# Kernel optimization log

Hardware: AMD Instinct MI355X
Metric: run time of the kernel (lower is better)

The kernel has to match this reference:

```python
import jax, jax.numpy as jnp
import numpy as np

S, B, H, NH = 2048, 1, 2048, 16
HD = H // NH
ROTARY_BASE = 10000.0
MASK_FILL = -10000.0  # gpt2_attention_mask_func fill value


def _rotate_half(x):
    x1, x2 = jnp.split(x, 2, axis=-1)
    return jnp.concatenate((-x2, x1), axis=-1)


def _rotary_cos_sin(seq_len, dim, dtype):
    inv_freq = 1.0 / (ROTARY_BASE ** (jnp.arange(0, dim, 2, dtype=jnp.float32) / dim))
    t = jnp.arange(seq_len, dtype=jnp.float32)
    freqs = t[:, None] * inv_freq[None, :]          # [s, dim/2]
    emb = jnp.concatenate((freqs, freqs), axis=-1)  # [s, dim]
    # shape [s, 1, 1, dim] to broadcast over (batch, heads)
    return jnp.cos(emb)[:, None, None, :].astype(dtype), jnp.sin(emb)[:, None, None, :].astype(dtype)


def setup_inputs() -> dict:
    key = jax.random.key(0)
    k0, k1, k2 = jax.random.split(key, 3)
    hidden_states = jax.random.normal(k0, (S, B, H), dtype=jnp.float32) * 0.02
    # causal mask: True = masked (upper triangle above diagonal)
    attention_mask = jnp.triu(jnp.ones((1, 1, S, S), dtype=bool), k=1)
    w_qkv = jax.random.normal(k1, (3 * H, H), dtype=jnp.float32) * 0.02
    b_qkv = jnp.zeros((3 * H,), dtype=jnp.float32)
    w_dense = jax.random.normal(k2, (H, H), dtype=jnp.float32) * 0.02
    return {"hidden_states": hidden_states, "attention_mask": attention_mask,
            "w_qkv": w_qkv, "b_qkv": b_qkv, "w_dense": w_dense}


def reference(hidden_states, attention_mask, w_qkv, b_qkv, w_dense):
    s, b, h = hidden_states.shape
    # fused QKV projection: [s, b, 3h]
    mixed = jnp.einsum('sbh,oh->sbo', hidden_states, w_qkv) + b_qkv
    mixed = mixed.reshape(s, b, NH, 3 * HD)
    q, k, v = jnp.split(mixed, 3, axis=-1)  # each [s, b, nh, hd]
    # rotary embedding (rotary_pct == 1 -> full head dim)
    cos, sin = _rotary_cos_sin(s, HD, q.dtype)
    q = q * cos + _rotate_half(q) * sin
    k = k * cos + _rotate_half(k) * sin
    # scaled QK^T: [b, nh, sq, sk]
    norm_factor = jnp.asarray(1.0 / np.sqrt(HD), dtype=q.dtype)
    scores = jnp.einsum('sbnd,tbnd->bnst', q, k) * norm_factor
    scores = jnp.where(attention_mask, jnp.asarray(MASK_FILL, scores.dtype), scores)
    probs = jax.nn.softmax(scores.astype(jnp.float32), axis=-1).astype(scores.dtype)
    # PV: [s, b, nh, hd]
    ctx = jnp.einsum('bnst,tbnd->sbnd', probs, v)
    ctx = ctx.reshape(s, b, h)
    # RowParallelLinear with skip_bias_add: bias returned separately (not added)
    out = jnp.einsum('sbh,oh->sbo', ctx, w_dense)
    return out
```

## Files before the change

### kernel.cpp

```cpp
#include <hip/hip_runtime.h>


#define S_LEN 2048
#define NHEAD 16
#define HDIM  128
#define HID   2048
#define H3    6144

typedef short bf16x8 __attribute__((ext_vector_type(8)));
typedef float f32x4  __attribute__((ext_vector_type(4)));

__device__ __forceinline__ float bf2f(ushort u) {
  union { float f; unsigned int i; } v; v.i = ((unsigned int)u) << 16; return v.f;
}
__device__ __forceinline__ ushort f2bf(float f) {
  union { float f; unsigned int i; } v; v.f = f;
  unsigned int r = v.i + 0x7fffu + ((v.i >> 16) & 1u);
  return (ushort)(r >> 16);
}
__device__ __forceinline__ int4 cvt8(const float* p) {
  float4 a = *(const float4*)p, b = *(const float4*)(p + 4);
  union { ushort u[8]; int4 v; } r;
  r.u[0] = f2bf(a.x); r.u[1] = f2bf(a.y); r.u[2] = f2bf(a.z); r.u[3] = f2bf(a.w);
  r.u[4] = f2bf(b.x); r.u[5] = f2bf(b.y); r.u[6] = f2bf(b.z); r.u[7] = f2bf(b.w);
  return r.v;
}

typedef __attribute__((address_space(1))) const unsigned int gu32;
typedef __attribute__((address_space(3))) unsigned int lu32;
__device__ __forceinline__ void async16(const void* g, void* l) {
  __builtin_amdgcn_global_load_lds((gu32*)g, (lu32*)l, 16, 0, 0);
}

__global__ __launch_bounds__(256) void cvt_bf16(const float* __restrict__ src,
                                                ushort* __restrict__ dst, int n8) {
  int i = blockIdx.x * 256 + threadIdx.x;
  if (i < n8) *(int4*)&dst[(size_t)i * 8] = cvt8(&src[(size_t)i * 8]);
}

template<int BM, int BN, bool HAS_BIAS, bool OUT_F32>
__global__ __launch_bounds__(256) void gemm_async(const ushort* __restrict__ A,
                                                  const ushort* __restrict__ W,
                                                  const float* __restrict__ bias,
                                                  void* __restrict__ Cv,
                                                  int N, int K, int AS, int AH) {
  __shared__ __align__(16) ushort As[BM * 32];
  __shared__ __align__(16) ushort Ws[BN * 32];
  const int tid  = threadIdx.x;
  const int lane = tid & 63;
  const int w    = tid >> 6;
  const int wr   = w >> 1, wc = w & 1;
  const int quad = lane >> 4, ln15 = lane & 15;
  const int tm = blockIdx.y * BM, tn = blockIdx.x * BN;
  constexpr int MI = BM / 32, NJ = BN / 32;

  f32x4 acc[MI][NJ];
#pragma unroll
  for (int i = 0; i < MI; ++i)
#pragma unroll
    for (int j = 0; j < NJ; ++j) acc[i][j] = (f32x4){0.f, 0.f, 0.f, 0.f};

  const int lrow = lane >> 2;
  const int lcol = (lane & 3) * 8;

  for (int k0 = 0; k0 < K; k0 += 32) {
    const int aoff = (k0 >> 7) * AH + (k0 & 127) + lcol;
    for (int r = w; r < (BM + BN) / 16; r += 4) {
      if (r < BM / 16) {
        async16(&A[(size_t)(tm + r * 16 + lrow) * AS + aoff], &As[r * 16 * 32]);
      } else {
        const int rb = r - BM / 16;
        async16(&W[(size_t)(tn + rb * 16 + lrow) * K + k0 + lcol], &Ws[rb * 16 * 32]);
      }
    }
    __syncthreads();
    bf16x8 af[MI], bw[NJ];
#pragma unroll
    for (int i = 0; i < MI; ++i)
      af[i] = *(const bf16x8*)&As[((BM / 2) * wr + 16 * i + ln15) * 32 + quad * 8];
#pragma unroll
    for (int j = 0; j < NJ; ++j)
      bw[j] = *(const bf16x8*)&Ws[((BN / 2) * wc + 16 * j + ln15) * 32 + quad * 8];
#pragma unroll
    for (int i = 0; i < MI; ++i)
#pragma unroll
      for (int j = 0; j < NJ; ++j)
        acc[i][j] = __builtin_amdgcn_mfma_f32_16x16x32_bf16(af[i], bw[j], acc[i][j], 0, 0, 0);
    __syncthreads();
  }

#pragma unroll
  for (int i = 0; i < MI; ++i)
#pragma unroll
    for (int j = 0; j < NJ; ++j) {
      int col = tn + (BN / 2) * wc + 16 * j + ln15;
      float badd = HAS_BIAS ? bias[col] : 0.0f;
#pragma unroll
      for (int r = 0; r < 4; ++r) {
        int row = tm + (BM / 2) * wr + 16 * i + 4 * quad + r;
        float val = acc[i][j][r] + badd;
        if (OUT_F32) ((float*)Cv)[(size_t)row * N + col] = val;
        else         ((ushort*)Cv)[(size_t)row * N + col] = f2bf(val);
      }
    }
}

template<bool A_F32, bool HAS_BIAS, bool OUT_F32>
__global__ __launch_bounds__(256) void gemm_bt(const void* __restrict__ Av,
                                               const float* __restrict__ W,
                                               const float* __restrict__ bias,
                                               void* __restrict__ Cv,
                                               int M, int N, int K, int AS, int AH) {
  __shared__ __align__(16) ushort As[128 * 40];
  __shared__ __align__(16) ushort Ws[128 * 40];
  const int tid  = threadIdx.x;
  const int lane = tid & 63;
  const int w    = tid >> 6;
  const int wr   = w >> 1, wc = w & 1;
  const int quad = lane >> 4, ln15 = lane & 15;
  const int tm = blockIdx.y * 128, tn = blockIdx.x * 128;

  f32x4 acc[4][4];
#pragma unroll
  for (int i = 0; i < 4; ++i)
#pragma unroll
    for (int j = 0; j < 4; ++j) acc[i][j] = (f32x4){0.f, 0.f, 0.f, 0.f};

  const int row0 = tid >> 2, row1 = row0 + 64;
  const int kp   = (tid & 3) * 8;

  for (int k0 = 0; k0 < K; k0 += 32) {
    const int ka   = k0 + kp;
    const int aoff = (ka >> 7) * AH + (ka & 127);
    if (A_F32) {
      const float* A = (const float*)Av;
      *(int4*)&As[row0 * 40 + kp] = cvt8(&A[(size_t)(tm + row0) * AS + aoff]);
      *(int4*)&As[row1 * 40 + kp] = cvt8(&A[(size_t)(tm + row1) * AS + aoff]);
    } else {
      const ushort* A = (const ushort*)Av;
      *(int4*)&As[row0 * 40 + kp] = *(const int4*)&A[(size_t)(tm + row0) * AS + aoff];
      *(int4*)&As[row1 * 40 + kp] = *(const int4*)&A[(size_t)(tm + row1) * AS + aoff];
    }
    *(int4*)&Ws[row0 * 40 + kp] = cvt8(&W[(size_t)(tn + row0) * K + ka]);
    *(int4*)&Ws[row1 * 40 + kp] = cvt8(&W[(size_t)(tn + row1) * K + ka]);
    __syncthreads();
    bf16x8 af[4], bw[4];
#pragma unroll
    for (int i = 0; i < 4; ++i)
      af[i] = *(const bf16x8*)&As[(64 * wr + 16 * i + ln15) * 40 + quad * 8];
#pragma unroll
    for (int j = 0; j < 4; ++j)
      bw[j] = *(const bf16x8*)&Ws[(64 * wc + 16 * j + ln15) * 40 + quad * 8];
#pragma unroll
    for (int i = 0; i < 4; ++i)
#pragma unroll
      for (int j = 0; j < 4; ++j)
        acc[i][j] = __builtin_amdgcn_mfma_f32_16x16x32_bf16(af[i], bw[j], acc[i][j], 0, 0, 0);
    __syncthreads();
  }

#pragma unroll
  for (int i = 0; i < 4; ++i)
#pragma unroll
    for (int j = 0; j < 4; ++j) {
      int col = tn + 64 * wc + 16 * j + ln15;
      float badd = HAS_BIAS ? bias[col] : 0.0f;
#pragma unroll
      for (int r = 0; r < 4; ++r) {
        int row = tm + 64 * wr + 16 * i + 4 * quad + r;
        float val = acc[i][j][r] + badd;
        if (OUT_F32) ((float*)Cv)[(size_t)row * N + col] = val;
        else         ((ushort*)Cv)[(size_t)row * N + col] = f2bf(val);
      }
    }
}

__global__ __launch_bounds__(256) void rope_kernel(ushort* __restrict__ mixed) {
  int t = blockIdx.x * 256 + threadIdx.x;
  int d = t & 63;
  int n = (t >> 6) & (NHEAD - 1);
  int s = t >> 10;
  ushort* base = mixed + (size_t)s * H3 + n * 384;
  float invf = exp2f((float)d * (-13.287712379549449f / 64.0f));
  float ang = (float)s * invf;
  float si, c; sincosf(ang, &si, &c);
  float q0 = bf2f(base[d]),       q1 = bf2f(base[64 + d]);
  float k0 = bf2f(base[128 + d]), k1 = bf2f(base[192 + d]);
  base[d]       = f2bf(q0 * c - q1 * si);
  base[64 + d]  = f2bf(q1 * c + q0 * si);
  base[128 + d] = f2bf(k0 * c - k1 * si);
  base[192 + d] = f2bf(k1 * c + k0 * si);
}

__global__ __launch_bounds__(256) void v_transpose(const ushort* __restrict__ mixed,
                                                   ushort* __restrict__ vt) {
  __shared__ __align__(16) ushort Vl[64 * 136];
  const int tid = threadIdx.x;
  const int sb = blockIdx.x;
  const int n  = blockIdx.y;
#pragma unroll
  for (int it = 0; it < 4; ++it) {
    int c = tid + it * 256;
    int row = c >> 4, dp = (c & 15) * 8;
    *(int4*)&Vl[row * 136 + dp] =
        *(const int4*)&mixed[(size_t)(sb * 64 + row) * H3 + n * 384 + 256 + dp];
  }
  __syncthreads();
#pragma unroll
  for (int it = 0; it < 4; ++it) {
    int c = tid + it * 256;
    int d = c >> 3, sp = (c & 7) * 8;
    union { ushort u[8]; int4 v; } pk;
#pragma unroll
    for (int e = 0; e < 8; ++e) pk.u[e] = Vl[(sp + e) * 136 + d];
    *(int4*)&vt[((size_t)(n * 128 + d)) * S_LEN + sb * 64 + sp] = pk.v;
  }
}

__global__ __launch_bounds__(256, 2) void attn_kernel(const ushort* __restrict__ mixed,
                                                      const ushort* __restrict__ vt,
                                                      ushort* __restrict__ ctx,
                                                      int CS, int CH) {
  __shared__ __align__(16) ushort Ks[2][64 * 128];
  __shared__ __align__(16) ushort Vs[128 * 64];
  __shared__ __align__(16) ushort Ss[4][16 * 72];

  const int tid  = threadIdx.x;
  const int lane = tid & 63;
  const int w    = tid >> 6;
  const int quad = lane >> 4, ln15 = lane & 15;
  const int qb = blockIdx.x;
  const int n  = blockIdx.y;
  const float scale = 0.08838834764831845f;

  const ushort* Kg = mixed + n * 384 + 128;
  const ushort* Vg = vt + (size_t)n * 128 * S_LEN;

  bf16x8 aqr[4];
#pragma unroll
  for (int ks = 0; ks < 4; ++ks)
    aqr[ks] = *(const bf16x8*)&mixed[(size_t)(qb * 64 + 16 * w + ln15) * H3 + n * 384
                                     + ks * 32 + quad * 8];

  f32x4 acc_o[8];
#pragma unroll
  for (int jt = 0; jt < 8; ++jt) acc_o[jt] = (f32x4){0.f, 0.f, 0.f, 0.f};
  float m_run[4], l_run[4];
#pragma unroll
  for (int r = 0; r < 4; ++r) { m_run[r] = -1e30f; l_run[r] = 0.0f; }

  ushort* Ssw = Ss[w];

  const int krow = lane >> 4, kcs = lane & 15;
  const int vrow = lane >> 3, vcs = lane & 7;
  const int swz  = ln15 & 7;

#define STAGE_K(KT, BUF)                                                        \
  { _Pragma("unroll")                                                           \
    for (int i = 0; i < 4; ++i) {                                               \
      int kr = w * 16 + i * 4 + krow;                                           \
      int kcl = kcs ^ (kr & 7);                                                 \
      async16(&Kg[(size_t)((KT) * 64 + kr) * H3 + kcl * 8],                     \
              &Ks[BUF][(w * 16 + i * 4) * 128]);                                \
    } }
#define STAGE_V(KT)                                                             \
  { _Pragma("unroll")                                                           \
    for (int i = 0; i < 4; ++i) {                                               \
      int vr = w * 32 + i * 8 + vrow;                                           \
      int vcl = vcs ^ (vr & 7);                                                 \
      async16(&Vg[(size_t)vr * S_LEN + (KT) * 64 + vcl * 8],                    \
              &Vs[(w * 32 + i * 8) * 64]);                                      \
    } }

  int cur = 0;
  STAGE_K(0, 0);
  __syncthreads();

  for (int kt = 0; kt <= qb; ++kt) {
    STAGE_V(kt);
    if (kt < qb) STAGE_K(kt + 1, cur ^ 1);

    f32x4 sacc[4];
#pragma unroll
    for (int jt = 0; jt < 4; ++jt) sacc[jt] = (f32x4){0.f, 0.f, 0.f, 0.f};
#pragma unroll
    for (int ks = 0; ks < 4; ++ks) {
#pragma unroll
      for (int jt = 0; jt < 4; ++jt) {
        bf16x8 bk = *(const bf16x8*)&Ks[cur][(16 * jt + ln15) * 128
                                            + ((ks * 4 + quad) ^ swz) * 8];
        sacc[jt] = __builtin_amdgcn_mfma_f32_16x16x32_bf16(aqr[ks], bk, sacc[jt], 0, 0, 0);
      }
    }

    float sv[4][4];
    const int ig = qb * 64 + 16 * w + 4 * quad;
#pragma unroll
    for (int jt = 0; jt < 4; ++jt) {
      int jg = kt * 64 + 16 * jt + ln15;
#pragma unroll
      for (int r = 0; r < 4; ++r) {
        float x = sacc[jt][r] * scale;
        sv[jt][r] = (jg > ig + r) ? -10000.0f : x;
      }
    }

    float tmx[4];
#pragma unroll
    for (int r = 0; r < 4; ++r)
      tmx[r] = fmaxf(fmaxf(sv[0][r], sv[1][r]), fmaxf(sv[2][r], sv[3][r]));
#pragma unroll
    for (int m = 1; m <= 8; m <<= 1)
#pragma unroll
      for (int r = 0; r < 4; ++r) tmx[r] = fmaxf(tmx[r], __shfl_xor(tmx[r], m));

    float alpha[4];
#pragma unroll
    for (int r = 0; r < 4; ++r) {
      float m_new = fmaxf(m_run[r], tmx[r]);
      alpha[r] = __expf(m_run[r] - m_new);
      m_run[r] = m_new;
    }

    float ps[4] = {0.f, 0.f, 0.f, 0.f};
#pragma unroll
    for (int jt = 0; jt < 4; ++jt)
#pragma unroll
      for (int r = 0; r < 4; ++r) {
        float p = __expf(sv[jt][r] - m_run[r]);
        Ssw[(4 * quad + r) * 72 + 16 * jt + ln15] = f2bf(p);
        ps[r] += p;
      }
#pragma unroll
    for (int m = 1; m <= 8; m <<= 1)
#pragma unroll
      for (int r = 0; r < 4; ++r) ps[r] += __shfl_xor(ps[r], m);
#pragma unroll
    for (int r = 0; r < 4; ++r) l_run[r] = alpha[r] * l_run[r] + ps[r];

#pragma unroll
    for (int jt = 0; jt < 8; ++jt)
#pragma unroll
      for (int r = 0; r < 4; ++r) acc_o[jt][r] *= alpha[r];

    __syncthreads();

#pragma unroll
    for (int ks = 0; ks < 2; ++ks) {
      bf16x8 ap = *(const bf16x8*)&Ssw[ln15 * 72 + ks * 32 + quad * 8];
#pragma unroll
      for (int jt = 0; jt < 8; ++jt) {
        bf16x8 bv = *(const bf16x8*)&Vs[(16 * jt + ln15) * 64
                                        + ((ks * 4 + quad) ^ swz) * 8];
        acc_o[jt] = __builtin_amdgcn_mfma_f32_16x16x32_bf16(ap, bv, acc_o[jt], 0, 0, 0);
      }
    }

    __syncthreads();
    cur ^= 1;
  }
#undef STAGE_K
#undef STAGE_V

  float rinv[4];
#pragma unroll
  for (int r = 0; r < 4; ++r) rinv[r] = 1.0f / l_run[r];
#pragma unroll
  for (int jt = 0; jt < 8; ++jt)
#pragma unroll
    for (int r = 0; r < 4; ++r) {
      int row = qb * 64 + 16 * w + 4 * quad + r;
      int col = 16 * jt + ln15;
      ctx[(size_t)row * CS + n * CH + col] = f2bf(acc_o[jt][r] * rinv[r]);
    }
}

extern "C" void kernel_launch(void* const* d_in, const int* in_sizes, int n_in,
                              void* d_out, int out_size, void* d_ws, size_t ws_size,
                              hipStream_t stream) {
  const float* hidden  = (const float*)d_in[0];
  const float* w_qkv   = (const float*)d_in[2];
  const float* b_qkv   = (const float*)d_in[3];
  const float* w_dense = (const float*)d_in[4];
  float* out = (float*)d_out;

  char* ws = (char*)d_ws;

  const size_t wq_b    = (size_t)H3 * HID * 2;
  const size_t h_b     = (size_t)S_LEN * HID * 2;
  const size_t mixed_b = (size_t)S_LEN * H3 * 2;
  const size_t vt_b    = (size_t)NHEAD * HDIM * S_LEN * 2;
  const size_t fast_need = wq_b + h_b + mixed_b + vt_b;

  if (ws_size >= fast_need) {
    ushort* WQ    = (ushort*)ws;
    ushort* Hbf   = (ushort*)(ws + wq_b);
    ushort* mixed = (ushort*)(ws + wq_b + h_b);
    ushort* vt    = (ushort*)(ws + wq_b + h_b + mixed_b);
    ushort* WD    = WQ;
    ushort* ctx   = mixed;

    cvt_bf16<<<2048, 256, 0, stream>>>(hidden, Hbf, S_LEN * HID / 8);
    cvt_bf16<<<6144, 256, 0, stream>>>(w_qkv, WQ, H3 * HID / 8);
    gemm_async<128, 128, true, false><<<dim3(48, 16), 256, 0, stream>>>(
        Hbf, WQ, b_qkv, mixed, H3, HID, HID, 128);
    rope_kernel<<<8192, 256, 0, stream>>>(mixed);
    v_transpose<<<dim3(32, 16), 256, 0, stream>>>(mixed, vt);
    attn_kernel<<<dim3(32, 16), 256, 0, stream>>>(mixed, vt, ctx, H3, 384);
    cvt_bf16<<<2048, 256, 0, stream>>>(w_dense, WD, HID * HID / 8);
    gemm_async<64, 128, false, true><<<dim3(16, 32), 256, 0, stream>>>(
        ctx, WD, nullptr, out, HID, HID, H3, 384);
  } else {
    ushort* mixed = (ushort*)ws;
    ushort* vt    = (ushort*)(ws + mixed_b);
    const bool big = ws_size >= mixed_b + vt_b + (size_t)S_LEN * HID * 2;
    ushort* ctx = big ? (ushort*)(ws + mixed_b + vt_b) : mixed;
    const int CS = big ? HID  : H3;
    const int CH = big ? HDIM : 384;

    gemm_bt<true, true, false><<<dim3(48, 16), 256, 0, stream>>>(
        hidden, w_qkv, b_qkv, mixed, S_LEN, H3, HID, HID, HDIM);
    rope_kernel<<<8192, 256, 0, stream>>>(mixed);
    v_transpose<<<dim3(32, 16), 256, 0, stream>>>(mixed, vt);
    attn_kernel<<<dim3(32, 16), 256, 0, stream>>>(mixed, vt, ctx, CS, CH);
    gemm_bt<false, false, true><<<dim3(16, 16), 256, 0, stream>>>(
        ctx, w_dense, nullptr, out, S_LEN, HID, HID, CS, CH);
  }
}
```

Measured before the change: 345.1 us.

## Keep attention probabilities in registers via transposed QK MFMA and permuted K rows

The QK^T MFMA now computes S^T by swapping its operands, and K rows are staged into shared memory in a permuted order. Each lane's score outputs then match the A-operand layout that the PV MFMA expects. This removes the per-wave shared-memory P buffer, its bf16 stores and reloads, and the 16-lane shuffle reductions; each query row is now reduced with two shuffles instead. Launch bounds are raised to 3 blocks per SM to use the freed LDS and registers, at the cost of extra __shfl calls for alpha and l and tighter register limits that could cause spills.

```diff
diff --git a/kernel.cpp b/kernel.cpp
--- a/kernel.cpp
+++ b/kernel.cpp
@@ -217,13 +217,12 @@
   }
 }
 
-__global__ __launch_bounds__(256, 2) void attn_kernel(const ushort* __restrict__ mixed,
+__global__ __launch_bounds__(256, 3) void attn_kernel(const ushort* __restrict__ mixed,
                                                       const ushort* __restrict__ vt,
                                                       ushort* __restrict__ ctx,
                                                       int CS, int CH) {
   __shared__ __align__(16) ushort Ks[2][64 * 128];
   __shared__ __align__(16) ushort Vs[128 * 64];
-  __shared__ __align__(16) ushort Ss[4][16 * 72];
 
   const int tid  = threadIdx.x;
   const int lane = tid & 63;
@@ -245,11 +244,7 @@
   f32x4 acc_o[8];
 #pragma unroll
   for (int jt = 0; jt < 8; ++jt) acc_o[jt] = (f32x4){0.f, 0.f, 0.f, 0.f};
-  float m_run[4], l_run[4];
-#pragma unroll
-  for (int r = 0; r < 4; ++r) { m_run[r] = -1e30f; l_run[r] = 0.0f; }
-
-  ushort* Ssw = Ss[w];
+  float m_run = -1e30f, l_run = 0.0f;
 
   const int krow = lane >> 4, kcs = lane & 15;
   const int vrow = lane >> 3, vcs = lane & 7;
@@ -258,9 +253,9 @@
 #define STAGE_K(KT, BUF)                                                        \
   { _Pragma("unroll")                                                           \
     for (int i = 0; i < 4; ++i) {                                               \
-      int kr = w * 16 + i * 4 + krow;                                           \
-      int kcl = kcs ^ (kr & 7);                                                 \
-      async16(&Kg[(size_t)((KT) * 64 + kr) * H3 + kcl * 8],                     \
+      int sig = ((w & 2) << 4) + 8 * i + ((w & 1) << 2) + krow;                 \
+      int kcl = kcs ^ ((i * 4 + krow) & 7);                                     \
+      async16(&Kg[(size_t)((KT) * 64 + sig) * H3 + kcl * 8],                    \
               &Ks[BUF][(w * 16 + i * 4) * 128]);                                \
     } }
 #define STAGE_V(KT)                                                             \
@@ -276,6 +271,8 @@
   STAGE_K(0, 0);
   __syncthreads();
 
+  const int ig = qb * 64 + 16 * w + ln15;
+
   for (int kt = 0; kt <= qb; ++kt) {
     STAGE_V(kt);
     if (kt < qb) STAGE_K(kt + 1, cur ^ 1);
@@ -289,71 +286,72 @@
       for (int jt = 0; jt < 4; ++jt) {
         bf16x8 bk = *(const bf16x8*)&Ks[cur][(16 * jt + ln15) * 128
                                             + ((ks * 4 + quad) ^ swz) * 8];
-        sacc[jt] = __builtin_amdgcn_mfma_f32_16x16x32_bf16(aqr[ks], bk, sacc[jt], 0, 0, 0);
+        sacc[jt] = __builtin_amdgcn_mfma_f32_16x16x32_bf16(bk, aqr[ks], sacc[jt], 0, 0, 0);
       }
     }
 
     float sv[4][4];
-    const int ig = qb * 64 + 16 * w + 4 * quad;
 #pragma unroll
     for (int jt = 0; jt < 4; ++jt) {
-      int jg = kt * 64 + 16 * jt + ln15;
 #pragma unroll
       for (int r = 0; r < 4; ++r) {
+        int kl = ((jt & 2) << 4) + 8 * quad + ((jt & 1) << 2) + r;
+        int jg = kt * 64 + kl;
         float x = sacc[jt][r] * scale;
-        sv[jt][r] = (jg > ig + r) ? -10000.0f : x;
-      }
-    }
-
-    float tmx[4];
-#pragma unroll
-    for (int r = 0; r < 4; ++r)
-      tmx[r] = fmaxf(fmaxf(sv[0][r], sv[1][r]), fmaxf(sv[2][r], sv[3][r]));
-#pragma unroll
-    for (int m = 1; m <= 8; m <<= 1)
-#pragma unroll
-      for (int r = 0; r < 4; ++r) tmx[r] = fmaxf(tmx[r], __shfl_xor(tmx[r], m));
-
-    float alpha[4];
-#pragma unroll
-    for (int r = 0; r < 4; ++r) {
-      float m_new = fmaxf(m_run[r], tmx[r]);
-      alpha[r] = __expf(m_run[r] - m_new);
-      m_run[r] = m_new;
-    }
-
-    float ps[4] = {0.f, 0.f, 0.f, 0.f};
+        sv[jt][r] = (jg > ig) ? -10000.0f : x;
+      }
+    }
+
+    float tmx = sv[0][0];
 #pragma unroll
     for (int jt = 0; jt < 4; ++jt)
 #pragma unroll
+      for (int r = 0; r < 4; ++r) tmx = fmaxf(tmx, sv[jt][r]);
+    tmx = fmaxf(tmx, __shfl_xor(tmx, 16));
+    tmx = fmaxf(tmx, __shfl_xor(tmx, 32));
+
+    float m_new = fmaxf(m_run, tmx);
+    float alpha = __expf(m_run - m_new);
+    m_run = m_new;
+
+    float p[4][4];
+    float ps = 0.0f;
+#pragma unroll
+    for (int jt = 0; jt < 4; ++jt)
+#pragma unroll
       for (int r = 0; r < 4; ++r) {
-        float p = __expf(sv[jt][r] - m_run[r]);
-        Ssw[(4 * quad + r) * 72 + 16 * jt + ln15] = f2bf(p);
-        ps[r] += p;
-      }
-#pragma unroll
-    for (int m = 1; m <= 8; m <<= 1)
-#pragma unroll
-      for (int r = 0; r < 4; ++r) ps[r] += __shfl_xor(ps[r], m);
-#pragma unroll
-    for (int r = 0; r < 4; ++r) l_run[r] = alpha[r] * l_run[r] + ps[r];
-
+        p[jt][r] = __expf(sv[jt][r] - m_run);
+        ps += p[jt][r];
+      }
+    ps += __shfl_xor(ps, 16);
+    ps += __shfl_xor(ps, 32);
+    l_run = alpha * l_run + ps;
+
+    float aw[4];
+#pragma unroll
+    for (int r = 0; r < 4; ++r) aw[r] = __shfl(alpha, 4 * quad + r);
 #pragma unroll
     for (int jt = 0; jt < 8; ++jt)
 #pragma unroll
-      for (int r = 0; r < 4; ++r) acc_o[jt][r] *= alpha[r];
-
-    __syncthreads();
-
-#pragma unroll
-    for (int ks = 0; ks < 2; ++ks) {
-      bf16x8 ap = *(const bf16x8*)&Ssw[ln15 * 72 + ks * 32 + quad * 8];
-#pragma unroll
-      for (int jt = 0; jt < 8; ++jt) {
-        bf16x8 bv = *(const bf16x8*)&Vs[(16 * jt + ln15) * 64
-                                        + ((ks * 4 + quad) ^ swz) * 8];
-        acc_o[jt] = __builtin_amdgcn_mfma_f32_16x16x32_bf16(ap, bv, acc_o[jt], 0, 0, 0);
-      }
+      for (int r = 0; r < 4; ++r) acc_o[jt][r] *= aw[r];
+
+    bf16x8 ap0, ap1;
+#pragma unroll
+    for (int j = 0; j < 4; ++j) {
+      ap0[j]     = (short)f2bf(p[0][j]);
+      ap0[4 + j] = (short)f2bf(p[1][j]);
+      ap1[j]     = (short)f2bf(p[2][j]);
+      ap1[4 + j] = (short)f2bf(p[3][j]);
+    }
+
+    __syncthreads();
+
+#pragma unroll
+    for (int jt = 0; jt < 8; ++jt) {
+      bf16x8 bv0 = *(const bf16x8*)&Vs[(16 * jt + ln15) * 64 + ((quad) ^ swz) * 8];
+      acc_o[jt] = __builtin_amdgcn_mfma_f32_16x16x32_bf16(ap0, bv0, acc_o[jt], 0, 0, 0);
+      bf16x8 bv1 = *(const bf16x8*)&Vs[(16 * jt + ln15) * 64 + ((4 + quad) ^ swz) * 8];
+      acc_o[jt] = __builtin_amdgcn_mfma_f32_16x16x32_bf16(ap1, bv1, acc_o[jt], 0, 0, 0);
     }
 
     __syncthreads();
@@ -364,7 +362,7 @@
 
   float rinv[4];
 #pragma unroll
-  for (int r = 0; r < 4; ++r) rinv[r] = 1.0f / l_run[r];
+  for (int r = 0; r < 4; ++r) rinv[r] = 1.0f / __shfl(l_run, 4 * quad + r);
 #pragma unroll
   for (int jt = 0; jt < 8; ++jt)
 #pragma unroll
```

After: 323.7 us. 6.2% less time.
